# Performance work log

Hardware: AMD Instinct MI355X
Metric: run time of the kernel (lower is better)

The kernel has to match this reference:

```python
import jax, jax.numpy as jnp
import numpy as np

SEQ_LEN = 1024
WINDOW = 32
NUM_HEADS = 16
BATCH = 8
DIM = 1024


def make_local_mask(seq_len=SEQ_LEN, window=WINDOW):
    # True = position is MASKED (disallowed), matching the torch bool attn_mask.
    # torch allows j in [i - window//2, i + window//2] inclusive.
    i = np.arange(seq_len)[:, None]
    j = np.arange(seq_len)[None, :]
    half = window // 2
    allowed = (j >= i - half) & (j <= i + half)
    return jnp.asarray(~allowed)


def setup_inputs() -> dict:
    key = jax.random.key(0)
    k_x, k_wi, k_wo = jax.random.split(key, 3)
    scale_in = 1.0 / np.sqrt(DIM)
    return {
        "x": jax.random.normal(k_x, (BATCH, SEQ_LEN, DIM), dtype=jnp.float32),
        "w_in": jax.random.normal(k_wi, (3 * DIM, DIM), dtype=jnp.float32) * scale_in,
        "b_in": jnp.zeros((3 * DIM,), dtype=jnp.float32),
        "w_out": jax.random.normal(k_wo, (DIM, DIM), dtype=jnp.float32) * scale_in,
        "b_out": jnp.zeros((DIM,), dtype=jnp.float32),
        "mask": make_local_mask(),
    }


def reference(x, w_in, b_in, w_out, b_out, mask):
    B, S, D = x.shape
    H = NUM_HEADS
    hd = D // H
    # fused in-projection (torch nn.MultiheadAttention self-attn path)
    qkv = x @ w_in.T + b_in                      # [B, S, 3D]
    q, k, v = jnp.split(qkv, 3, axis=-1)
    q = q.reshape(B, S, H, hd).transpose(0, 2, 1, 3)  # [B, H, S, hd]
    k = k.reshape(B, S, H, hd).transpose(0, 2, 1, 3)
    v = v.reshape(B, S, H, hd).transpose(0, 2, 1, 3)
    scores = jnp.einsum("bhqd,bhkd->bhqk", q, k) / jnp.sqrt(jnp.asarray(hd, x.dtype))
    neg = jnp.asarray(jnp.finfo(x.dtype).min, x.dtype)
    scores = jnp.where(mask[None, None, :, :], neg, scores)
    attn = jax.nn.softmax(scores, axis=-1)
    ctx = jnp.einsum("bhqk,bhkd->bhqd", attn, v)  # [B, H, S, hd]
    ctx = ctx.transpose(0, 2, 1, 3).reshape(B, S, D)
    return ctx @ w_out.T + b_out
```

## Files before the change

kernel.cpp:

```cpp
#include <hip/hip_runtime.h>

#define S_LEN   1024
#define NH      16
#define HD      64
#define BATCHN  8
#define DMODEL  1024
#define HALF_W  16

typedef __attribute__((ext_vector_type(8))) short bf16x8;
typedef __attribute__((ext_vector_type(4))) float f32x4;

__device__ __forceinline__ unsigned short f2bf(float f) {
  unsigned u = __builtin_bit_cast(unsigned, f);
  u += 0x7fffu + ((u >> 16) & 1u);
  return (unsigned short)(u >> 16);
}
__device__ __forceinline__ float bf2f(unsigned short h) {
  return __builtin_bit_cast(float, ((unsigned)h) << 16);
}

__device__ __forceinline__ void gload_lds16(const void* g, void* l) {
  __builtin_amdgcn_global_load_lds(
      (const __attribute__((address_space(1))) void*)g,
      (__attribute__((address_space(3))) void*)l, 16, 0, 0);
}

__global__ __launch_bounds__(256) void cvt_bf16_kernel(
    const float* __restrict__ in, unsigned short* __restrict__ out, int n4) {
  int t = blockIdx.x * 256 + threadIdx.x;
  if (t >= n4) return;
  float4 v = reinterpret_cast<const float4*>(in)[t];
  ushort4 o = make_ushort4(f2bf(v.x), f2bf(v.y), f2bf(v.z), f2bf(v.w));
  reinterpret_cast<ushort4*>(out)[t] = o;
}

#define MFMA_BF16 __builtin_amdgcn_mfma_f32_16x16x32_bf16

#define GATE(NSTR) do {                                                    \
    asm volatile("s_waitcnt vmcnt(" NSTR ")" ::: "memory");                \
    __builtin_amdgcn_sched_barrier(0);                                     \
    __builtin_amdgcn_s_barrier(); } while (0)

#define STAGE_A(KT, BUF, KH) do {                                          \
    gload_lds16(gA_s + (KT) * 64 + (KH) * 32,          &sA[BUF][KH][wid * 512]); \
    gload_lds16(gA_s + 131072 + (KT) * 64 + (KH) * 32, &sA[BUF][KH][wid * 512 + 4096]); } while (0)
#define STAGE_B(KT, BUF, KH) do {                                          \
    gload_lds16(gB_s + (KT) * 64 + (KH) * 32,          &sB[BUF][KH][wid * 512]); \
    gload_lds16(gB_s + 131072 + (KT) * 64 + (KH) * 32, &sB[BUF][KH][wid * 512 + 4096]); } while (0)

#define PH(BUF, KH, CH, STG) do {                                          \
    const unsigned short* _pa = &sA[BUF][KH][arow + (CH) * 2048];          \
    bf16x8 a0_ = *(const bf16x8*)(_pa);                                    \
    bf16x8 a1_ = *(const bf16x8*)(_pa + 512);                              \
    bf16x8 a2_ = *(const bf16x8*)(_pa + 1024);                             \
    bf16x8 a3_ = *(const bf16x8*)(_pa + 1536);                             \
    if ((CH) == 0) {                                                       \
      const unsigned short* _pb = &sB[BUF][KH][brow];                      \
      nb0 = *(const bf16x8*)(_pb);        nb1 = *(const bf16x8*)(_pb + 512);  \
      nb2 = *(const bf16x8*)(_pb + 1024); nb3 = *(const bf16x8*)(_pb + 1536); } \
    STG;                                                                   \
    asm volatile("s_waitcnt lgkmcnt(0)" ::: "memory");                     \
    __builtin_amdgcn_sched_barrier(0);                                     \
    __builtin_amdgcn_s_setprio(1);                                         \
    acc[(CH)*4+0][0] = MFMA_BF16(a0_, nb0, acc[(CH)*4+0][0], 0, 0, 0);     \
    acc[(CH)*4+0][1] = MFMA_BF16(a0_, nb1, acc[(CH)*4+0][1], 0, 0, 0);     \
    acc[(CH)*4+0][2] = MFMA_BF16(a0_, nb2, acc[(CH)*4+0][2], 0, 0, 0);     \
    acc[(CH)*4+0][3] = MFMA_BF16(a0_, nb3, acc[(CH)*4+0][3], 0, 0, 0);     \
    acc[(CH)*4+1][0] = MFMA_BF16(a1_, nb0, acc[(CH)*4+1][0], 0, 0, 0);     \
    acc[(CH)*4+1][1] = MFMA_BF16(a1_, nb1, acc[(CH)*4+1][1], 0, 0, 0);     \
    acc[(CH)*4+1][2] = MFMA_BF16(a1_, nb2, acc[(CH)*4+1][2], 0, 0, 0);     \
    acc[(CH)*4+1][3] = MFMA_BF16(a1_, nb3, acc[(CH)*4+1][3], 0, 0, 0);     \
    acc[(CH)*4+2][0] = MFMA_BF16(a2_, nb0, acc[(CH)*4+2][0], 0, 0, 0);     \
    acc[(CH)*4+2][1] = MFMA_BF16(a2_, nb1, acc[(CH)*4+2][1], 0, 0, 0);     \
    acc[(CH)*4+2][2] = MFMA_BF16(a2_, nb2, acc[(CH)*4+2][2], 0, 0, 0);     \
    acc[(CH)*4+2][3] = MFMA_BF16(a2_, nb3, acc[(CH)*4+2][3], 0, 0, 0);     \
    acc[(CH)*4+3][0] = MFMA_BF16(a3_, nb0, acc[(CH)*4+3][0], 0, 0, 0);     \
    acc[(CH)*4+3][1] = MFMA_BF16(a3_, nb1, acc[(CH)*4+3][1], 0, 0, 0);     \
    acc[(CH)*4+3][2] = MFMA_BF16(a3_, nb2, acc[(CH)*4+3][2], 0, 0, 0);     \
    acc[(CH)*4+3][3] = MFMA_BF16(a3_, nb3, acc[(CH)*4+3][3], 0, 0, 0);     \
    __builtin_amdgcn_s_setprio(0);                                         \
  } while (0)

template <int OUT_BF16>
__global__ __launch_bounds__(512, 2) void gemm256_kernel(
    const unsigned short* __restrict__ A,
    const unsigned short* __restrict__ B,
    const float* __restrict__ bias,
    void* __restrict__ Cv,
    int N, int gy) {
  __shared__ __align__(16) unsigned short sA[2][2][8192];
  __shared__ __align__(16) unsigned short sB[2][2][8192];

  const int tid  = threadIdx.x;
  const int lane = tid & 63;
  const int wid  = tid >> 6;
  const int wm   = wid >> 2;
  const int wn   = wid & 3;
  const int lgrp = lane >> 4;
  const int l15  = lane & 15;

  const int nwg = gridDim.x;
  const int cpx = nwg >> 3;
  const int sid = (blockIdx.x & 7) * cpx + (blockIdx.x >> 3);
  const int tileM = (sid / gy) * 256;
  const int tileN = (sid % gy) * 256;

  const int srow = tid >> 2;
  const int sk   = tid & 3;
  const int scol = (sk ^ ((srow & 3) ^ ((srow >> 2) & 3))) * 8;
  const unsigned short* gA_s = A + (size_t)(tileM + srow) * 1024 + scol;
  const unsigned short* gB_s = B + (size_t)(tileN + srow) * 1024 + scol;

  const int axr  = lgrp ^ ((l15 & 3) ^ ((l15 >> 2) & 3));
  const int arow = (wm * 128 + l15) * 32 + axr * 8;
  const int brow = (wn * 64  + l15) * 32 + axr * 8;

  f32x4 acc[8][4] = {};
  bf16x8 nb0 = {}, nb1 = {}, nb2 = {}, nb3 = {};

  STAGE_A(0, 0, 0); STAGE_B(0, 0, 0);
  STAGE_A(0, 0, 1); STAGE_B(0, 0, 1);
  STAGE_A(1, 1, 0); STAGE_B(1, 1, 0);

  for (int kt = 0; kt < 14; kt += 2) {
    GATE("8"); PH(0, 0, 0, STAGE_A(kt + 1, 1, 1));
               PH(0, 0, 1, STAGE_B(kt + 1, 1, 1));
    GATE("8"); PH(0, 1, 0, STAGE_A(kt + 2, 0, 0));
               PH(0, 1, 1, STAGE_B(kt + 2, 0, 0));
    GATE("8"); PH(1, 0, 0, STAGE_A(kt + 2, 0, 1));
               PH(1, 0, 1, STAGE_B(kt + 2, 0, 1));
    GATE("8"); PH(1, 1, 0, STAGE_A(kt + 3, 1, 0));
               PH(1, 1, 1, STAGE_B(kt + 3, 1, 0));
  }
  GATE("8"); PH(0, 0, 0, STAGE_A(15, 1, 1));
             PH(0, 0, 1, STAGE_B(15, 1, 1));
  GATE("8"); PH(0, 1, 0, (void)0);
             PH(0, 1, 1, (void)0);
  GATE("4"); PH(1, 0, 0, (void)0);
             PH(1, 0, 1, (void)0);
  GATE("0"); PH(1, 1, 0, (void)0);
             PH(1, 1, 1, (void)0);

#pragma unroll
  for (int nt = 0; nt < 4; ++nt) {
    const int col = tileN + wn * 64 + nt * 16 + l15;
    const float bs = bias[col];
#pragma unroll
    for (int ch = 0; ch < 2; ++ch)
#pragma unroll
      for (int mt = 0; mt < 4; ++mt) {
        const int row0 = tileM + wm * 128 + ch * 64 + mt * 16 + lgrp * 4;
#pragma unroll
        for (int rr = 0; rr < 4; ++rr) {
          float v = acc[ch * 4 + mt][nt][rr] + bs;
          if (OUT_BF16) {
            ((unsigned short*)Cv)[(size_t)(row0 + rr) * N + col] = f2bf(v);
          } else {
            ((float*)Cv)[(size_t)(row0 + rr) * N + col] = v;
          }
        }
      }
  }
}

#define KST 72
#define PST 104

__global__ __launch_bounds__(256) void attn_local_kernel(
    const unsigned short* __restrict__ qkv, unsigned short* __restrict__ ctx) {
  __shared__ __align__(16) unsigned short sKP[96 * KST];
  __shared__ __align__(16) unsigned short sQ[64 * KST];
  __shared__ __align__(16) unsigned short sVT[64 * PST];

  const int tid  = threadIdx.x;
  const int lane = tid & 63;
  const int wid  = tid >> 6;
  const int qc   = lane & 15;
  const int lgrp = lane >> 4;

  const int qb = blockIdx.x & 15;
  const int h  = (blockIdx.x >> 4) & 15;
  const int b  = blockIdx.x >> 8;
  const int i0 = qb * 64;

  const unsigned short* hb = qkv + (size_t)b * S_LEN * 3072 + (size_t)h * HD;

#pragma unroll
  for (int it = 0; it < 3; ++it) {
    int c  = it * 256 + tid;
    int r  = c >> 3;
    int d0 = (c & 7) * 8;
    int j  = i0 - 16 + r;
    bf16x8 kv = {}, vv = {};
    if (0 <= j && j < S_LEN) {
      const unsigned short* rp = hb + (size_t)j * 3072;
      kv = *reinterpret_cast<const bf16x8*>(rp + DMODEL + d0);
      vv = *reinterpret_cast<const bf16x8*>(rp + 2 * DMODEL + d0);
    }
    *reinterpret_cast<bf16x8*>(&sKP[r * KST + d0]) = kv;
#pragma unroll
    for (int jj = 0; jj < 8; ++jj) {
      int dd = (jj + c) & 7;
      sVT[(d0 + dd) * PST + r] = (unsigned short)vv[dd];
    }
  }
#pragma unroll
  for (int it = 0; it < 2; ++it) {
    int c  = it * 256 + tid;
    int r  = c >> 3;
    int d0 = (c & 7) * 8;
    bf16x8 qv = *reinterpret_cast<const bf16x8*>(hb + (size_t)(i0 + r) * 3072 + d0);
    *reinterpret_cast<bf16x8*>(&sQ[r * KST + d0]) = qv;
  }
  __syncthreads();

  const int q0 = wid * 16;

  bf16x8 bq[2];
#pragma unroll
  for (int ks = 0; ks < 2; ++ks)
    bq[ks] = *reinterpret_cast<const bf16x8*>(
        &sQ[(q0 + qc) * KST + ks * 32 + lgrp * 8]);

  f32x4 st[6] = {};
#pragma unroll
  for (int kt = 0; kt < 6; ++kt) {
#pragma unroll
    for (int ks = 0; ks < 2; ++ks) {
      bf16x8 fa = *reinterpret_cast<const bf16x8*>(
          &sKP[(kt * 16 + qc) * KST + ks * 32 + lgrp * 8]);
      st[kt] = __builtin_amdgcn_mfma_f32_16x16x32_bf16(fa, bq[ks], st[kt], 0, 0, 0);
    }
  }
  __syncthreads();

  const int q = q0 + qc;
  float pv[6][4];
  float mx = -3.0e38f;
#pragma unroll
  for (int kt = 0; kt < 6; ++kt)
#pragma unroll
    for (int rr = 0; rr < 4; ++rr) {
      int kk = kt * 16 + lgrp * 4 + rr;
      int j  = i0 - 16 + kk;
      bool ok = (j >= 0) && (j < S_LEN) && (kk >= q) && (kk <= q + 32);
      float s = ok ? st[kt][rr] * 0.125f : -3.0e38f;
      pv[kt][rr] = s;
      mx = fmaxf(mx, s);
    }
  mx = fmaxf(mx, __shfl_xor(mx, 16, 64));
  mx = fmaxf(mx, __shfl_xor(mx, 32, 64));

  float rsum = 0.f;
#pragma unroll
  for (int kt = 0; kt < 6; ++kt)
#pragma unroll
    for (int rr = 0; rr < 4; ++rr) {
      float p = __expf(pv[kt][rr] - mx);
      pv[kt][rr] = p;
      rsum += p;
    }
  rsum += __shfl_xor(rsum, 16, 64);
  rsum += __shfl_xor(rsum, 32, 64);
  const float inv = 1.0f / rsum;

  unsigned short* sP = sKP;
#pragma unroll
  for (int kt = 0; kt < 6; ++kt) {
    ushort4 w = make_ushort4(f2bf(pv[kt][0]), f2bf(pv[kt][1]),
                             f2bf(pv[kt][2]), f2bf(pv[kt][3]));
    *reinterpret_cast<ushort4*>(&sP[(q0 + qc) * PST + kt * 16 + lgrp * 4]) = w;
  }

  bf16x8 pb[3];
#pragma unroll
  for (int ks = 0; ks < 3; ++ks)
    pb[ks] = *reinterpret_cast<const bf16x8*>(
        &sP[(q0 + qc) * PST + ks * 32 + lgrp * 8]);

  f32x4 ct[4] = {};
#pragma unroll
  for (int dt = 0; dt < 4; ++dt)
#pragma unroll
    for (int ks = 0; ks < 3; ++ks) {
      bf16x8 fa = *reinterpret_cast<const bf16x8*>(
          &sVT[(dt * 16 + qc) * PST + ks * 32 + lgrp * 8]);
      ct[dt] = __builtin_amdgcn_mfma_f32_16x16x32_bf16(fa, pb[ks], ct[dt], 0, 0, 0);
    }

  unsigned short* op =
      ctx + ((size_t)b * S_LEN + i0 + q0 + qc) * DMODEL + h * HD;
#pragma unroll
  for (int dt = 0; dt < 4; ++dt) {
    ushort4 w = make_ushort4(
        f2bf(ct[dt][0] * inv), f2bf(ct[dt][1] * inv),
        f2bf(ct[dt][2] * inv), f2bf(ct[dt][3] * inv));
    *reinterpret_cast<ushort4*>(op + dt * 16 + lgrp * 4) = w;
  }
}

extern "C" void kernel_launch(void* const* d_in, const int* in_sizes, int n_in,
                              void* d_out, int out_size, void* d_ws, size_t ws_size,
                              hipStream_t stream) {
  const float* x     = (const float*)d_in[0];
  const float* w_in  = (const float*)d_in[1];
  const float* b_in  = (const float*)d_in[2];
  const float* w_out = (const float*)d_in[3];
  const float* b_out = (const float*)d_in[4];
  float* out = (float*)d_out;

  unsigned short* xb   = (unsigned short*)d_ws;
  unsigned short* wib  = xb  + (size_t)8192 * 1024;
  unsigned short* wob  = wib + (size_t)3072 * 1024;
  unsigned short* qkv  = wob + (size_t)1024 * 1024;
  unsigned short* ctxb = qkv + (size_t)8192 * 3072;

  cvt_bf16_kernel<<<8192, 256, 0, stream>>>(x, xb, (8192 * 1024) / 4);
  cvt_bf16_kernel<<<3072, 256, 0, stream>>>(w_in, wib, (3072 * 1024) / 4);
  cvt_bf16_kernel<<<1024, 256, 0, stream>>>(w_out, wob, (1024 * 1024) / 4);

  gemm256_kernel<1><<<384, 512, 0, stream>>>(
      xb, wib, b_in, (void*)qkv, 3072, 12);

  attn_local_kernel<<<BATCHN * NH * (S_LEN / 64), 256, 0, stream>>>(qkv, ctxb);

  gemm256_kernel<0><<<128, 512, 0, stream>>>(
      ctxb, wob, b_out, (void*)out, 1024, 4);
}
```

Measured before the change: 139.2 us.

## Template GEMM on M-tile height and use 128x256 tiles for out-projection

Generalizes the GEMM kernel with a CHN parameter that sets the M-tile height (128 or 256 rows). The out-projection now launches 256 workgroups of 128x256 tiles instead of 128 of 256x256, so more CUs have work on the smaller GEMM. The change also drops the XOR swizzle on LDS staging and reads, which may add LDS bank conflicts. It forces the main loop to stay rolled, which shrinks code but may cost scheduling freedom.

Measured after the change: 132.4 us. 4.8% less time.

```diff
diff --git a/kernel.cpp b/kernel.cpp
--- a/kernel.cpp
+++ b/kernel.cpp
@@ -36,17 +36,67 @@
 
 #define MFMA_BF16 __builtin_amdgcn_mfma_f32_16x16x32_bf16
 
-#define GATE(NSTR) do {                                                    \
-    asm volatile("s_waitcnt vmcnt(" NSTR ")" ::: "memory");                \
+template <int OUT_BF16, int CHN>
+__global__ __launch_bounds__(512, 2) void gemmdp_kernel(
+    const unsigned short* __restrict__ A,
+    const unsigned short* __restrict__ B,
+    const float* __restrict__ bias,
+    void* __restrict__ Cv,
+    int N, int gy) {
+  __shared__ __align__(16) unsigned short sA[2][2][CHN * 4096];
+  __shared__ __align__(16) unsigned short sB[2][2][8192];
+
+  const int tid  = threadIdx.x;
+  const int lane = tid & 63;
+  const int wid  = tid >> 6;
+  const int wm   = wid >> 2;
+  const int wn   = wid & 3;
+  const int lgrp = lane >> 4;
+  const int l15  = lane & 15;
+
+  const int nwg = gridDim.x;
+  const int cpx = nwg >> 3;
+  const int sid = (blockIdx.x & 7) * cpx + (blockIdx.x >> 3);
+  const int tileM = (sid / gy) * (CHN * 128);
+  const int tileN = (sid % gy) * 256;
+
+  const int srow = tid >> 2;
+  const int scol = (tid & 3) * 8;
+  const unsigned short* gA_s = A + (size_t)(tileM + srow) * 1024 + scol;
+  const unsigned short* gB_s = B + (size_t)(tileN + srow) * 1024 + scol;
+
+  const int arow = (wm * (CHN * 64) + l15) * 32 + lgrp * 8;
+  const int brow = (wn * 64 + l15) * 32 + lgrp * 8;
+
+  f32x4 acc[CHN * 4][4] = {};
+  bf16x8 nb0 = {}, nb1 = {}, nb2 = {}, nb3 = {};
+
+#define SSA(KT, BUF, KH) do {                                              \
+    const unsigned short* _sa = gA_s + (KT) * 64 + (KH) * 32;              \
+    gload_lds16(_sa, &sA[BUF][KH][wid * 512]);                             \
+    if constexpr (CHN == 2)                                                \
+      gload_lds16(_sa + 131072, &sA[BUF][KH][4096 + wid * 512]);           \
+  } while (0)
+#define SSB(KT, BUF, KH) do {                                              \
+    const unsigned short* _sb = gB_s + (KT) * 64 + (KH) * 32;              \
+    gload_lds16(_sb, &sB[BUF][KH][wid * 512]);                             \
+    gload_lds16(_sb + 131072, &sB[BUF][KH][4096 + wid * 512]);             \
+  } while (0)
+
+#define GATE_S do {                                                        \
+    if constexpr (CHN == 2) asm volatile("s_waitcnt vmcnt(8)" ::: "memory");\
+    else                    asm volatile("s_waitcnt vmcnt(6)" ::: "memory");\
     __builtin_amdgcn_sched_barrier(0);                                     \
     __builtin_amdgcn_s_barrier(); } while (0)
-
-#define STAGE_A(KT, BUF, KH) do {                                          \
-    gload_lds16(gA_s + (KT) * 64 + (KH) * 32,          &sA[BUF][KH][wid * 512]); \
-    gload_lds16(gA_s + 131072 + (KT) * 64 + (KH) * 32, &sA[BUF][KH][wid * 512 + 4096]); } while (0)
-#define STAGE_B(KT, BUF, KH) do {                                          \
-    gload_lds16(gB_s + (KT) * 64 + (KH) * 32,          &sB[BUF][KH][wid * 512]); \
-    gload_lds16(gB_s + 131072 + (KT) * 64 + (KH) * 32, &sB[BUF][KH][wid * 512 + 4096]); } while (0)
+#define GATE_H do {                                                        \
+    if constexpr (CHN == 2) asm volatile("s_waitcnt vmcnt(4)" ::: "memory");\
+    else                    asm volatile("s_waitcnt vmcnt(3)" ::: "memory");\
+    __builtin_amdgcn_sched_barrier(0);                                     \
+    __builtin_amdgcn_s_barrier(); } while (0)
+#define GATE_Z do {                                                        \
+    asm volatile("s_waitcnt vmcnt(0)" ::: "memory");                       \
+    __builtin_amdgcn_sched_barrier(0);                                     \
+    __builtin_amdgcn_s_barrier(); } while (0)
 
 #define PH(BUF, KH, CH, STG) do {                                          \
     const unsigned short* _pa = &sA[BUF][KH][arow + (CH) * 2048];          \
@@ -81,75 +131,49 @@
     __builtin_amdgcn_s_setprio(0);                                         \
   } while (0)
 
-template <int OUT_BF16>
-__global__ __launch_bounds__(512, 2) void gemm256_kernel(
-    const unsigned short* __restrict__ A,
-    const unsigned short* __restrict__ B,
-    const float* __restrict__ bias,
-    void* __restrict__ Cv,
-    int N, int gy) {
-  __shared__ __align__(16) unsigned short sA[2][2][8192];
-  __shared__ __align__(16) unsigned short sB[2][2][8192];
-
-  const int tid  = threadIdx.x;
-  const int lane = tid & 63;
-  const int wid  = tid >> 6;
-  const int wm   = wid >> 2;
-  const int wn   = wid & 3;
-  const int lgrp = lane >> 4;
-  const int l15  = lane & 15;
-
-  const int nwg = gridDim.x;
-  const int cpx = nwg >> 3;
-  const int sid = (blockIdx.x & 7) * cpx + (blockIdx.x >> 3);
-  const int tileM = (sid / gy) * 256;
-  const int tileN = (sid % gy) * 256;
-
-  const int srow = tid >> 2;
-  const int sk   = tid & 3;
-  const int scol = (sk ^ ((srow & 3) ^ ((srow >> 2) & 3))) * 8;
-  const unsigned short* gA_s = A + (size_t)(tileM + srow) * 1024 + scol;
-  const unsigned short* gB_s = B + (size_t)(tileN + srow) * 1024 + scol;
-
-  const int axr  = lgrp ^ ((l15 & 3) ^ ((l15 >> 2) & 3));
-  const int arow = (wm * 128 + l15) * 32 + axr * 8;
-  const int brow = (wn * 64  + l15) * 32 + axr * 8;
-
-  f32x4 acc[8][4] = {};
-  bf16x8 nb0 = {}, nb1 = {}, nb2 = {}, nb3 = {};
-
-  STAGE_A(0, 0, 0); STAGE_B(0, 0, 0);
-  STAGE_A(0, 0, 1); STAGE_B(0, 0, 1);
-  STAGE_A(1, 1, 0); STAGE_B(1, 1, 0);
-
+#define DOPAIR(BUF, KH, STGA, STGB) do {                                   \
+    if constexpr (CHN == 2) {                                              \
+      PH(BUF, KH, 0, STGA);                                                \
+      PH(BUF, KH, 1, STGB);                                                \
+    } else {                                                               \
+      PH(BUF, KH, 0, do { STGA; STGB; } while (0));                        \
+    } } while (0)
+#define NOSTG ((void)0)
+
+  SSA(0, 0, 0); SSB(0, 0, 0);
+  SSA(0, 0, 1); SSB(0, 0, 1);
+  SSA(1, 1, 0); SSB(1, 1, 0);
+
+#pragma unroll 1
   for (int kt = 0; kt < 14; kt += 2) {
-    GATE("8"); PH(0, 0, 0, STAGE_A(kt + 1, 1, 1));
-               PH(0, 0, 1, STAGE_B(kt + 1, 1, 1));
-    GATE("8"); PH(0, 1, 0, STAGE_A(kt + 2, 0, 0));
-               PH(0, 1, 1, STAGE_B(kt + 2, 0, 0));
-    GATE("8"); PH(1, 0, 0, STAGE_A(kt + 2, 0, 1));
-               PH(1, 0, 1, STAGE_B(kt + 2, 0, 1));
-    GATE("8"); PH(1, 1, 0, STAGE_A(kt + 3, 1, 0));
-               PH(1, 1, 1, STAGE_B(kt + 3, 1, 0));
-  }
-  GATE("8"); PH(0, 0, 0, STAGE_A(15, 1, 1));
-             PH(0, 0, 1, STAGE_B(15, 1, 1));
-  GATE("8"); PH(0, 1, 0, (void)0);
-             PH(0, 1, 1, (void)0);
-  GATE("4"); PH(1, 0, 0, (void)0);
-             PH(1, 0, 1, (void)0);
-  GATE("0"); PH(1, 1, 0, (void)0);
-             PH(1, 1, 1, (void)0);
+    GATE_S; DOPAIR(0, 0, SSA(kt + 1, 1, 1), SSB(kt + 1, 1, 1));
+    GATE_S; DOPAIR(0, 1, SSA(kt + 2, 0, 0), SSB(kt + 2, 0, 0));
+    GATE_S; DOPAIR(1, 0, SSA(kt + 2, 0, 1), SSB(kt + 2, 0, 1));
+    GATE_S; DOPAIR(1, 1, SSA(kt + 3, 1, 0), SSB(kt + 3, 1, 0));
+  }
+  GATE_S; DOPAIR(0, 0, SSA(15, 1, 1), SSB(15, 1, 1));
+  GATE_S; DOPAIR(0, 1, NOSTG, NOSTG);
+  GATE_H; DOPAIR(1, 0, NOSTG, NOSTG);
+  GATE_Z; DOPAIR(1, 1, NOSTG, NOSTG);
+
+#undef SSA
+#undef SSB
+#undef GATE_S
+#undef GATE_H
+#undef GATE_Z
+#undef PH
+#undef DOPAIR
+#undef NOSTG
 
 #pragma unroll
   for (int nt = 0; nt < 4; ++nt) {
     const int col = tileN + wn * 64 + nt * 16 + l15;
     const float bs = bias[col];
 #pragma unroll
-    for (int ch = 0; ch < 2; ++ch)
+    for (int ch = 0; ch < CHN; ++ch)
 #pragma unroll
       for (int mt = 0; mt < 4; ++mt) {
-        const int row0 = tileM + wm * 128 + ch * 64 + mt * 16 + lgrp * 4;
+        const int row0 = tileM + wm * (CHN * 64) + ch * 64 + mt * 16 + lgrp * 4;
 #pragma unroll
         for (int rr = 0; rr < 4; ++rr) {
           float v = acc[ch * 4 + mt][nt][rr] + bs;
@@ -319,11 +343,11 @@
   cvt_bf16_kernel<<<3072, 256, 0, stream>>>(w_in, wib, (3072 * 1024) / 4);
   cvt_bf16_kernel<<<1024, 256, 0, stream>>>(w_out, wob, (1024 * 1024) / 4);
 
-  gemm256_kernel<1><<<384, 512, 0, stream>>>(
+  gemmdp_kernel<1, 2><<<384, 512, 0, stream>>>(
       xb, wib, b_in, (void*)qkv, 3072, 12);
 
   attn_local_kernel<<<BATCHN * NH * (S_LEN / 64), 256, 0, stream>>>(qkv, ctxb);
 
-  gemm256_kernel<0><<<128, 512, 0, stream>>>(
+  gemmdp_kernel<0, 1><<<256, 512, 0, stream>>>(
       ctxb, wob, b_out, (void*)out, 1024, 4);
 }
```
